# Performance work log

Hardware: AMD Instinct MI355X
Metric: run time of the kernel (lower is better)

The kernel has to match this reference:

```python
import jax, jax.numpy as jnp
import numpy as np

N_FFT = 1024
HOP = 256
WIN = 1024
PAD = (WIN - HOP) // 2  # 'same' padding trim
B, NBINS, T = 32, N_FFT // 2 + 1, 2048


def setup_inputs() -> dict:
    key = jax.random.key(0)
    k1, k2 = jax.random.split(key)
    spec_real = jax.random.normal(k1, (B, NBINS, T), dtype=jnp.float32)
    spec_imag = jax.random.normal(k2, (B, NBINS, T), dtype=jnp.float32)
    # Hann window, as used by neural vocoders (periodic hann)
    n = jnp.arange(WIN, dtype=jnp.float32)
    window = 0.5 - 0.5 * jnp.cos(2.0 * jnp.pi * n / WIN)
    return {"spec_real": spec_real, "spec_imag": spec_imag, "window": window}


def reference(spec_real, spec_imag, window):
    spec = jax.lax.complex(spec_real, spec_imag)            # (B, N, T)
    ifft = jnp.fft.irfft(spec, n=N_FFT, axis=1, norm="backward")  # (B, n_fft, T)
    ifft = ifft * window[None, :, None]                     # windowed frames
    b, _, t = spec_real.shape
    out_size = (t - 1) * HOP + WIN
    idx = jnp.arange(t)[None, :] * HOP + jnp.arange(WIN)[:, None]
    y = jnp.zeros((b, out_size), dtype=ifft.dtype).at[:, idx].add(ifft)
    env = jnp.zeros((out_size,), dtype=window.dtype).at[idx].add(
        jnp.broadcast_to(jnp.square(window)[:, None], (WIN, t))
    )
    return y[:, PAD:-PAD] / env[PAD:-PAD]
```

## Files before the change

kernel.cpp:

```cpp
#include <hip/hip_runtime.h>
#include <hip/hip_fp16.h>

#define NBINS 513
#define TFR   2048
#define NB    32
#define WIN   1024
#define HOP   256
#define PADT  384
#define OPB   524288
#define FR    8
#define TILES (TFR / FR)
#define FSTRIDE 545
#define PIDX(i) ((i) + ((i) >> 4))
#define C45 0.70710678118654752f
#define TWOPI_1024 0.0061359231515425649f
#define SSC   (1.0f / 512.0f * 2.0f / 3.0f)
#define CDLT  0.99998117528260114f
#define SDLT  0.00613588464915448f

__device__ __forceinline__ float2 cadd(float2 a, float2 b){ return make_float2(a.x+b.x, a.y+b.y); }
__device__ __forceinline__ float2 csub(float2 a, float2 b){ return make_float2(a.x-b.x, a.y-b.y); }
__device__ __forceinline__ float2 cmul(float2 a, float2 b){ return make_float2(a.x*b.x - a.y*b.y, a.x*b.y + a.y*b.x); }

__device__ __forceinline__ float2 h2f(__half2 h){ return __half22float2(h); }
__device__ __forceinline__ __half2 f2h(float x, float y){ return __floats2half2_rn(x, y); }

#define BFLY8(u0,u1,u2,u3,u4,u5,u6,u7, v0,v1,v2,v3,v4,v5,v6,v7)            \
    float2 s0=cadd(u0,u4), t0=csub(u0,u4);                                  \
    float2 s1=cadd(u1,u5), t1=csub(u1,u5);                                  \
    float2 s2=cadd(u2,u6), t2=csub(u2,u6);                                  \
    float2 s3=cadd(u3,u7), t3=csub(u3,u7);                                  \
    t1 = make_float2(C45*(t1.x - t1.y),  C45*(t1.x + t1.y));                \
    t2 = make_float2(-t2.y, t2.x);                                          \
    t3 = make_float2(-C45*(t3.x + t3.y), C45*(t3.x - t3.y));                \
    float2 p0=cadd(s0,s2), p2=csub(s0,s2);                                  \
    float2 p1=cadd(s1,s3), p3=csub(s1,s3); p3 = make_float2(-p3.y, p3.x);   \
    float2 q0=cadd(t0,t2), q2=csub(t0,t2);                                  \
    float2 q1=cadd(t1,t3), q3=csub(t1,t3); q3 = make_float2(-q3.y, q3.x);   \
    float2 v0=cadd(p0,p1), v4=csub(p0,p1);                                  \
    float2 v2=cadd(p2,p3), v6=csub(p2,p3);                                  \
    float2 v1=cadd(q0,q1), v5=csub(q0,q1);                                  \
    float2 v3=cadd(q2,q3), v7=csub(q2,q3);

template<int L>
__device__ __forceinline__ void fft_stage(__half2* __restrict__ row,
                                          const float2* __restrict__ ph, int i)
{
    const int k    = i & (L - 1);
    const int base = ((i & ~(L - 1)) << 3) + k;
    float2 u0 = h2f(row[PIDX(base + 0*L)]);
    float2 u1 = h2f(row[PIDX(base + 1*L)]);
    float2 u2 = h2f(row[PIDX(base + 2*L)]);
    float2 u3 = h2f(row[PIDX(base + 3*L)]);
    float2 u4 = h2f(row[PIDX(base + 4*L)]);
    float2 u5 = h2f(row[PIDX(base + 5*L)]);
    float2 u6 = h2f(row[PIDX(base + 6*L)]);
    float2 u7 = h2f(row[PIDX(base + 7*L)]);
    BFLY8(u0,u1,u2,u3,u4,u5,u6,u7, v0,v1,v2,v3,v4,v5,v6,v7)
    if constexpr (L > 1) {
        const float2 w1 = ph[k * (128 / L)];
        float2 wq = w1;
        v1 = cmul(v1, wq);
        wq = cmul(wq, w1); v2 = cmul(v2, wq);
        wq = cmul(wq, w1); v3 = cmul(v3, wq);
        wq = cmul(wq, w1); v4 = cmul(v4, wq);
        wq = cmul(wq, w1); v5 = cmul(v5, wq);
        wq = cmul(wq, w1); v6 = cmul(v6, wq);
        wq = cmul(wq, w1); v7 = cmul(v7, wq);
    }
    row[PIDX(base + 0*L)] = f2h(v0.x, v0.y);
    row[PIDX(base + 1*L)] = f2h(v1.x, v1.y);
    row[PIDX(base + 2*L)] = f2h(v2.x, v2.y);
    row[PIDX(base + 3*L)] = f2h(v3.x, v3.y);
    row[PIDX(base + 4*L)] = f2h(v4.x, v4.y);
    row[PIDX(base + 5*L)] = f2h(v5.x, v5.y);
    row[PIDX(base + 6*L)] = f2h(v6.x, v6.y);
    row[PIDX(base + 7*L)] = f2h(v7.x, v7.y);
}

__device__ __forceinline__ float2 hann_pair(const float2* __restrict__ ph, int n)
{
    const bool mir = n > 256;
    const int  m   = mir ? 512 - n : n;
    const float2 cs = ph[m];
    const float c = mir ? -cs.x : cs.x;
    const float s = cs.y;
    const float w0 = 1.0f - c*c;
    const float c2 = 2.0f*c*c - 1.0f;
    const float s2 = 2.0f*c*s;
    const float w1 = 0.5f - 0.5f*(c2*CDLT - s2*SDLT);
    return make_float2(w0, w1);
}

__global__ __launch_bounds__(256) void zero_seams(float* __restrict__ out)
{
    const int total = NB * 257 * 768;
    for (int id = blockIdx.x * 256 + threadIdx.x; id < total; id += gridDim.x * 256) {
        const int q = id % 768;
        const int r = id / 768;
        const int s = r % 257;
        const int bb = r / 257;
        const int p  = s * 2048 + q;
        const int oi = p - PADT;
        if ((unsigned)oi < (unsigned)OPB) out[(size_t)bb * OPB + oi] = 0.f;
    }
}

__global__ __launch_bounds__(256, 8) void istft8(
    const float* __restrict__ sr, const float* __restrict__ si,
    float* __restrict__ out)
{
    __shared__ __half2 stile[FR * FSTRIDE];
    __shared__ float2  ph[257];

    const int tid = threadIdx.x;
    const int bid = blockIdx.x;
    const int nwg = NB * TILES;
    const int swz = (bid & 7) * (nwg >> 3) + (bid >> 3);
    const int b    = swz / TILES;
    const int tile = swz % TILES;
    const int j0   = tile * FR;

    for (int m = tid; m < 257; m += 256) {
        float sv, cv;
        sincosf(TWOPI_1024 * (float)m, &sv, &cv);
        ph[m] = make_float2(cv, sv);
    }

    const size_t gbase = (size_t)b * NBINS * TFR + (size_t)j0;
    const size_t gaA = gbase + (size_t)tid * TFR;
    const size_t gaB = gbase + (size_t)(512 - tid) * TFR;
    float4 reA0 = *(const float4*)(sr + gaA);
    float4 reA1 = *(const float4*)(sr + gaA + 4);
    float4 imA0 = *(const float4*)(si + gaA);
    float4 imA1 = *(const float4*)(si + gaA + 4);
    float4 reB0 = *(const float4*)(sr + gaB);
    float4 reB1 = *(const float4*)(sr + gaB + 4);
    float4 imB0 = *(const float4*)(si + gaB);
    float4 imB1 = *(const float4*)(si + gaB + 4);
    float4 reC0, reC1, imC0, imC1;
    if (tid == 0) {
        imA0 = imA1 = imB0 = imB1 = make_float4(0.f,0.f,0.f,0.f);
        const size_t gaC = gbase + (size_t)256 * TFR;
        reC0 = *(const float4*)(sr + gaC);
        reC1 = *(const float4*)(sr + gaC + 4);
        imC0 = *(const float4*)(si + gaC);
        imC1 = *(const float4*)(si + gaC + 4);
    }
    __syncthreads();

    {
        const float h = 0.5f * SSC;
        const float2 wt = ph[tid];
        const int pk  = PIDX(tid);
        const int pk2 = PIDX(512 - tid);
#define TRICK(F, XKX, XKY, XMX, XMY) do {                                   \
            const float Ex = h*((XKX)+(XMX)), Ey = h*((XKY)-(XMY));         \
            const float Dx = h*((XKX)-(XMX)), Dy = h*((XKY)+(XMY));         \
            const float Ox = Dx*wt.x - Dy*wt.y, Oy = Dx*wt.y + Dy*wt.x;     \
            stile[(F)*FSTRIDE + pk]  = f2h(Ex - Oy, Ey + Ox);               \
            stile[(F)*FSTRIDE + pk2] = f2h(Ex + Oy, Ox - Ey);               \
        } while (0)
        TRICK(0, reA0.x, imA0.x, reB0.x, imB0.x);
        TRICK(1, reA0.y, imA0.y, reB0.y, imB0.y);
        TRICK(2, reA0.z, imA0.z, reB0.z, imB0.z);
        TRICK(3, reA0.w, imA0.w, reB0.w, imB0.w);
        TRICK(4, reA1.x, imA1.x, reB1.x, imB1.x);
        TRICK(5, reA1.y, imA1.y, reB1.y, imB1.y);
        TRICK(6, reA1.z, imA1.z, reB1.z, imB1.z);
        TRICK(7, reA1.w, imA1.w, reB1.w, imB1.w);
#undef TRICK
        if (tid == 0) {
            const int pn = PIDX(256);
            stile[0*FSTRIDE + pn] = f2h(reC0.x * SSC, -imC0.x * SSC);
            stile[1*FSTRIDE + pn] = f2h(reC0.y * SSC, -imC0.y * SSC);
            stile[2*FSTRIDE + pn] = f2h(reC0.z * SSC, -imC0.z * SSC);
            stile[3*FSTRIDE + pn] = f2h(reC0.w * SSC, -imC0.w * SSC);
            stile[4*FSTRIDE + pn] = f2h(reC1.x * SSC, -imC1.x * SSC);
            stile[5*FSTRIDE + pn] = f2h(reC1.y * SSC, -imC1.y * SSC);
            stile[6*FSTRIDE + pn] = f2h(reC1.z * SSC, -imC1.z * SSC);
            stile[7*FSTRIDE + pn] = f2h(reC1.w * SSC, -imC1.w * SSC);
        }
    }
    __syncthreads();

    {
        const int f  = tid >> 5;
        __half2* row = &stile[f * FSTRIDE];
        const int i0 = tid & 31;
        fft_stage<64>(row, ph, i0);
        fft_stage<64>(row, ph, i0 + 32);
        __syncthreads();
        fft_stage<8>(row, ph, i0);
        fft_stage<8>(row, ph, i0 + 32);
        __syncthreads();
        fft_stage<1>(row, ph, i0);
        fft_stage<1>(row, ph, i0 + 32);
        __syncthreads();
    }

    const int nE = tid;
    const int nO = (tid + 128) & 255;
    const float2 wE0 = hann_pair(ph, nE);
    const float2 wE1 = hann_pair(ph, nE + 256);
    const float2 wO0 = hann_pair(ph, nO);
    const float2 wO1 = hann_pair(ph, nO + 256);

    float2 a0 = make_float2(0.f,0.f), a1 = a0, a2 = a0, a3 = a0, a4 = a0, a5 = a0;
    const bool tlo = (tid < 128);

#define OLA_STEP(F, KK, ACCV, W) do {                                       \
        const int n_ = (((F) & 1) ? nO : nE) + ((KK) << 8);                 \
        const int j_ = ((n_ & 7) << 6) | (n_ & 56) | (n_ >> 6);             \
        const float2 z_ = h2f(stile[(F)*FSTRIDE + PIDX(j_)]);               \
        ACCV.x += z_.x * W.x;                                               \
        ACCV.y += z_.y * W.y;                                               \
    } while (0)

    OLA_STEP(0,0,a0,wE0); OLA_STEP(0,1,a1,wE1);
    if (tlo) { OLA_STEP(1,0,a1,wO0); OLA_STEP(1,1,a2,wO1); }
    else     { OLA_STEP(1,0,a0,wO0); OLA_STEP(1,1,a1,wO1); }
    OLA_STEP(2,0,a1,wE0); OLA_STEP(2,1,a2,wE1);
    if (tlo) { OLA_STEP(3,0,a2,wO0); OLA_STEP(3,1,a3,wO1); }
    else     { OLA_STEP(3,0,a1,wO0); OLA_STEP(3,1,a2,wO1); }
    OLA_STEP(4,0,a2,wE0); OLA_STEP(4,1,a3,wE1);
    if (tlo) { OLA_STEP(5,0,a3,wO0); OLA_STEP(5,1,a4,wO1); }
    else     { OLA_STEP(5,0,a2,wO0); OLA_STEP(5,1,a3,wO1); }
    OLA_STEP(6,0,a3,wE0); OLA_STEP(6,1,a4,wE1);
    if (tlo) { OLA_STEP(7,0,a4,wO0); OLA_STEP(7,1,a5,wO1); }
    else     { OLA_STEP(7,0,a3,wO0); OLA_STEP(7,1,a4,wO1); }
#undef OLA_STEP

    const size_t ob = (size_t)b * OPB;
    const int pb = tile * 2048;
#define STORE_SEAM(A, G) do {                                               \
        const int oi_ = pb + 2*(tid + 256*(G)) - PADT;                      \
        if ((unsigned)oi_ < (unsigned)OPB)       atomicAdd(&out[ob + oi_],     A.x); \
        if ((unsigned)(oi_+1) < (unsigned)OPB)   atomicAdd(&out[ob + oi_ + 1], A.y); \
    } while (0)
#define STORE_PLAIN(A, G) do {                                              \
        const int oi_ = pb + 2*(tid + 256*(G)) - PADT;                      \
        *(float2*)(out + ob + oi_) = A;                                     \
    } while (0)

    STORE_SEAM(a0, 0);
    if (tlo) STORE_SEAM(a1, 1);
    else     STORE_PLAIN(a1, 1);
    STORE_PLAIN(a2, 2);
    STORE_PLAIN(a3, 3);
    STORE_SEAM(a4, 4);
    if (tlo) STORE_SEAM(a5, 5);
#undef STORE_SEAM
#undef STORE_PLAIN
}

__global__ __launch_bounds__(256) void edge_fix(float* __restrict__ out)
{
    const int id = blockIdx.x * 256 + threadIdx.x;
    if (id >= 768 * NB) return;
    const int bb = id / 768;
    const int r  = id % 768;
    const int oi = (r < 384) ? r : (OPB - 768 + r);
    const int p  = oi + PADT;
    int jlo = (p - 768) >> 8; if (jlo < 0) jlo = 0;
    int jhi = p >> 8;         if (jhi > TFR - 1) jhi = TFR - 1;
    float e = 0.f;
    for (int j = jlo; j <= jhi; ++j) {
        const float wv = 0.5f - 0.5f * cosf(TWOPI_1024 * (float)(p - j * HOP));
        e += wv * wv;
    }
    out[(size_t)bb * OPB + oi] *= 1.5f / e;
}

extern "C" void kernel_launch(void* const* d_in, const int* in_sizes, int n_in,
                              void* d_out, int out_size, void* d_ws, size_t ws_size,
                              hipStream_t stream) {
    const float* sr = (const float*)d_in[0];
    const float* si = (const float*)d_in[1];
    float* out = (float*)d_out;

    hipLaunchKernelGGL(zero_seams, dim3(2048), dim3(256), 0, stream, out);
    hipLaunchKernelGGL(istft8, dim3(NB * TILES), dim3(256), 0, stream, sr, si, out);
    hipLaunchKernelGGL(edge_fix, dim3((768 * NB + 255) / 256), dim3(256), 0, stream, out);
}
```

Baseline: 134.4 us.

## Process 16 frames per block to halve seam atomics and tile count

Each workgroup now handles 16 STFT frames instead of 8. The input loads, FFT stage loops and overlap-add chain are extended, and zero_seams and the store pattern are updated so that only the tile boundaries use atomics. The twiddle for the pre-FFT trick is computed with sincosf per thread rather than read from shared memory, which lets the first barrier be dropped. The intent is fewer seam atomicAdds, less seam zeroing and less per-block overhead, at the cost of doubled LDS and registers per block (launch bounds drop to 4 blocks per SM) and twice the per-thread FFT work.

```diff
diff --git a/kernel.cpp b/kernel.cpp
--- a/kernel.cpp
+++ b/kernel.cpp
@@ -8,8 +8,9 @@
 #define HOP   256
 #define PADT  384
 #define OPB   524288
-#define FR    8
+#define FR    16
 #define TILES (TFR / FR)
+#define SPAN  (FR * HOP)
 #define FSTRIDE 545
 #define PIDX(i) ((i) + ((i) >> 4))
 #define C45 0.70710678118654752f
@@ -21,7 +22,6 @@
 __device__ __forceinline__ float2 cadd(float2 a, float2 b){ return make_float2(a.x+b.x, a.y+b.y); }
 __device__ __forceinline__ float2 csub(float2 a, float2 b){ return make_float2(a.x-b.x, a.y-b.y); }
 __device__ __forceinline__ float2 cmul(float2 a, float2 b){ return make_float2(a.x*b.x - a.y*b.y, a.x*b.y + a.y*b.x); }
-
 __device__ __forceinline__ float2 h2f(__half2 h){ return __half22float2(h); }
 __device__ __forceinline__ __half2 f2h(float x, float y){ return __floats2half2_rn(x, y); }
 
@@ -94,19 +94,19 @@
 
 __global__ __launch_bounds__(256) void zero_seams(float* __restrict__ out)
 {
-    const int total = NB * 257 * 768;
+    const int total = NB * (TILES + 1) * 768;
     for (int id = blockIdx.x * 256 + threadIdx.x; id < total; id += gridDim.x * 256) {
         const int q = id % 768;
         const int r = id / 768;
-        const int s = r % 257;
-        const int bb = r / 257;
-        const int p  = s * 2048 + q;
+        const int s = r % (TILES + 1);
+        const int bb = r / (TILES + 1);
+        const int p  = s * SPAN + q;
         const int oi = p - PADT;
         if ((unsigned)oi < (unsigned)OPB) out[(size_t)bb * OPB + oi] = 0.f;
     }
 }
 
-__global__ __launch_bounds__(256, 8) void istft8(
+__global__ __launch_bounds__(256, 4) void istft16(
     const float* __restrict__ sr, const float* __restrict__ si,
     float* __restrict__ out)
 {
@@ -121,81 +121,104 @@
     const int tile = swz % TILES;
     const int j0   = tile * FR;
 
+    const size_t gbase = (size_t)b * NBINS * TFR + (size_t)j0;
+    const size_t gaA = gbase + (size_t)tid * TFR;
+    const size_t gaB = gbase + (size_t)(512 - tid) * TFR;
+    float4 rA0 = *(const float4*)(sr + gaA);
+    float4 rA1 = *(const float4*)(sr + gaA + 4);
+    float4 rA2 = *(const float4*)(sr + gaA + 8);
+    float4 rA3 = *(const float4*)(sr + gaA + 12);
+    float4 iA0 = *(const float4*)(si + gaA);
+    float4 iA1 = *(const float4*)(si + gaA + 4);
+    float4 iA2 = *(const float4*)(si + gaA + 8);
+    float4 iA3 = *(const float4*)(si + gaA + 12);
+    float4 rB0 = *(const float4*)(sr + gaB);
+    float4 rB1 = *(const float4*)(sr + gaB + 4);
+    float4 rB2 = *(const float4*)(sr + gaB + 8);
+    float4 rB3 = *(const float4*)(sr + gaB + 12);
+    float4 iB0 = *(const float4*)(si + gaB);
+    float4 iB1 = *(const float4*)(si + gaB + 4);
+    float4 iB2 = *(const float4*)(si + gaB + 8);
+    float4 iB3 = *(const float4*)(si + gaB + 12);
+
+    if (tid == 0) {
+        const float4 z4 = make_float4(0.f,0.f,0.f,0.f);
+        iA0=iA1=iA2=iA3=z4; iB0=iB1=iB2=iB3=z4;
+        const size_t gaC = gbase + (size_t)256 * TFR;
+        float4 rC0 = *(const float4*)(sr + gaC);
+        float4 rC1 = *(const float4*)(sr + gaC + 4);
+        float4 rC2 = *(const float4*)(sr + gaC + 8);
+        float4 rC3 = *(const float4*)(sr + gaC + 12);
+        float4 iC0 = *(const float4*)(si + gaC);
+        float4 iC1 = *(const float4*)(si + gaC + 4);
+        float4 iC2 = *(const float4*)(si + gaC + 8);
+        float4 iC3 = *(const float4*)(si + gaC + 12);
+        const int pn = PIDX(256);
+#define Z256(F, RC, IC, COMP) stile[(F)*FSTRIDE + pn] = f2h(RC.COMP * SSC, -IC.COMP * SSC)
+        Z256(0,rC0,iC0,x);  Z256(1,rC0,iC0,y);  Z256(2,rC0,iC0,z);  Z256(3,rC0,iC0,w);
+        Z256(4,rC1,iC1,x);  Z256(5,rC1,iC1,y);  Z256(6,rC1,iC1,z);  Z256(7,rC1,iC1,w);
+        Z256(8,rC2,iC2,x);  Z256(9,rC2,iC2,y);  Z256(10,rC2,iC2,z); Z256(11,rC2,iC2,w);
+        Z256(12,rC3,iC3,x); Z256(13,rC3,iC3,y); Z256(14,rC3,iC3,z); Z256(15,rC3,iC3,w);
+#undef Z256
+    }
+
     for (int m = tid; m < 257; m += 256) {
         float sv, cv;
         sincosf(TWOPI_1024 * (float)m, &sv, &cv);
         ph[m] = make_float2(cv, sv);
     }
 
-    const size_t gbase = (size_t)b * NBINS * TFR + (size_t)j0;
-    const size_t gaA = gbase + (size_t)tid * TFR;
-    const size_t gaB = gbase + (size_t)(512 - tid) * TFR;
-    float4 reA0 = *(const float4*)(sr + gaA);
-    float4 reA1 = *(const float4*)(sr + gaA + 4);
-    float4 imA0 = *(const float4*)(si + gaA);
-    float4 imA1 = *(const float4*)(si + gaA + 4);
-    float4 reB0 = *(const float4*)(sr + gaB);
-    float4 reB1 = *(const float4*)(sr + gaB + 4);
-    float4 imB0 = *(const float4*)(si + gaB);
-    float4 imB1 = *(const float4*)(si + gaB + 4);
-    float4 reC0, reC1, imC0, imC1;
-    if (tid == 0) {
-        imA0 = imA1 = imB0 = imB1 = make_float4(0.f,0.f,0.f,0.f);
-        const size_t gaC = gbase + (size_t)256 * TFR;
-        reC0 = *(const float4*)(sr + gaC);
-        reC1 = *(const float4*)(sr + gaC + 4);
-        imC0 = *(const float4*)(si + gaC);
-        imC1 = *(const float4*)(si + gaC + 4);
-    }
-    __syncthreads();
-
     {
         const float h = 0.5f * SSC;
-        const float2 wt = ph[tid];
+        float swt, cwt;
+        sincosf(TWOPI_1024 * (float)tid, &swt, &cwt);
         const int pk  = PIDX(tid);
         const int pk2 = PIDX(512 - tid);
 #define TRICK(F, XKX, XKY, XMX, XMY) do {                                   \
             const float Ex = h*((XKX)+(XMX)), Ey = h*((XKY)-(XMY));         \
             const float Dx = h*((XKX)-(XMX)), Dy = h*((XKY)+(XMY));         \
-            const float Ox = Dx*wt.x - Dy*wt.y, Oy = Dx*wt.y + Dy*wt.x;     \
+            const float Ox = Dx*cwt - Dy*swt, Oy = Dx*swt + Dy*cwt;         \
             stile[(F)*FSTRIDE + pk]  = f2h(Ex - Oy, Ey + Ox);               \
             stile[(F)*FSTRIDE + pk2] = f2h(Ex + Oy, Ox - Ey);               \
         } while (0)
-        TRICK(0, reA0.x, imA0.x, reB0.x, imB0.x);
-        TRICK(1, reA0.y, imA0.y, reB0.y, imB0.y);
-        TRICK(2, reA0.z, imA0.z, reB0.z, imB0.z);
-        TRICK(3, reA0.w, imA0.w, reB0.w, imB0.w);
-        TRICK(4, reA1.x, imA1.x, reB1.x, imB1.x);
-        TRICK(5, reA1.y, imA1.y, reB1.y, imB1.y);
-        TRICK(6, reA1.z, imA1.z, reB1.z, imB1.z);
-        TRICK(7, reA1.w, imA1.w, reB1.w, imB1.w);
+        TRICK(0,  rA0.x, iA0.x, rB0.x, iB0.x);
+        TRICK(1,  rA0.y, iA0.y, rB0.y, iB0.y);
+        TRICK(2,  rA0.z, iA0.z, rB0.z, iB0.z);
+        TRICK(3,  rA0.w, iA0.w, rB0.w, iB0.w);
+        TRICK(4,  rA1.x, iA1.x, rB1.x, iB1.x);
+        TRICK(5,  rA1.y, iA1.y, rB1.y, iB1.y);
+        TRICK(6,  rA1.z, iA1.z, rB1.z, iB1.z);
+        TRICK(7,  rA1.w, iA1.w, rB1.w, iB1.w);
+        TRICK(8,  rA2.x, iA2.x, rB2.x, iB2.x);
+        TRICK(9,  rA2.y, iA2.y, rB2.y, iB2.y);
+        TRICK(10, rA2.z, iA2.z, rB2.z, iB2.z);
+        TRICK(11, rA2.w, iA2.w, rB2.w, iB2.w);
+        TRICK(12, rA3.x, iA3.x, rB3.x, iB3.x);
+        TRICK(13, rA3.y, iA3.y, rB3.y, iB3.y);
+        TRICK(14, rA3.z, iA3.z, rB3.z, iB3.z);
+        TRICK(15, rA3.w, iA3.w, rB3.w, iB3.w);
 #undef TRICK
-        if (tid == 0) {
-            const int pn = PIDX(256);
-            stile[0*FSTRIDE + pn] = f2h(reC0.x * SSC, -imC0.x * SSC);
-            stile[1*FSTRIDE + pn] = f2h(reC0.y * SSC, -imC0.y * SSC);
-            stile[2*FSTRIDE + pn] = f2h(reC0.z * SSC, -imC0.z * SSC);
-            stile[3*FSTRIDE + pn] = f2h(reC0.w * SSC, -imC0.w * SSC);
-            stile[4*FSTRIDE + pn] = f2h(reC1.x * SSC, -imC1.x * SSC);
-            stile[5*FSTRIDE + pn] = f2h(reC1.y * SSC, -imC1.y * SSC);
-            stile[6*FSTRIDE + pn] = f2h(reC1.z * SSC, -imC1.z * SSC);
-            stile[7*FSTRIDE + pn] = f2h(reC1.w * SSC, -imC1.w * SSC);
-        }
     }
     __syncthreads();
 
     {
-        const int f  = tid >> 5;
+        const int f  = tid >> 4;
         __half2* row = &stile[f * FSTRIDE];
-        const int i0 = tid & 31;
+        const int i0 = tid & 15;
         fft_stage<64>(row, ph, i0);
+        fft_stage<64>(row, ph, i0 + 16);
         fft_stage<64>(row, ph, i0 + 32);
+        fft_stage<64>(row, ph, i0 + 48);
         __syncthreads();
         fft_stage<8>(row, ph, i0);
+        fft_stage<8>(row, ph, i0 + 16);
         fft_stage<8>(row, ph, i0 + 32);
+        fft_stage<8>(row, ph, i0 + 48);
         __syncthreads();
         fft_stage<1>(row, ph, i0);
+        fft_stage<1>(row, ph, i0 + 16);
         fft_stage<1>(row, ph, i0 + 32);
+        fft_stage<1>(row, ph, i0 + 48);
         __syncthreads();
     }
 
@@ -206,7 +229,8 @@
     const float2 wO0 = hann_pair(ph, nO);
     const float2 wO1 = hann_pair(ph, nO + 256);
 
-    float2 a0 = make_float2(0.f,0.f), a1 = a0, a2 = a0, a3 = a0, a4 = a0, a5 = a0;
+    float2 a0 = make_float2(0.f,0.f), a1=a0, a2=a0, a3=a0, a4=a0,
+           a5 = a0, a6=a0, a7=a0, a8=a0, a9=a0;
     const bool tlo = (tid < 128);
 
 #define OLA_STEP(F, KK, ACCV, W) do {                                       \
@@ -217,22 +241,34 @@
         ACCV.y += z_.y * W.y;                                               \
     } while (0)
 
-    OLA_STEP(0,0,a0,wE0); OLA_STEP(0,1,a1,wE1);
-    if (tlo) { OLA_STEP(1,0,a1,wO0); OLA_STEP(1,1,a2,wO1); }
-    else     { OLA_STEP(1,0,a0,wO0); OLA_STEP(1,1,a1,wO1); }
-    OLA_STEP(2,0,a1,wE0); OLA_STEP(2,1,a2,wE1);
-    if (tlo) { OLA_STEP(3,0,a2,wO0); OLA_STEP(3,1,a3,wO1); }
-    else     { OLA_STEP(3,0,a1,wO0); OLA_STEP(3,1,a2,wO1); }
-    OLA_STEP(4,0,a2,wE0); OLA_STEP(4,1,a3,wE1);
-    if (tlo) { OLA_STEP(5,0,a3,wO0); OLA_STEP(5,1,a4,wO1); }
-    else     { OLA_STEP(5,0,a2,wO0); OLA_STEP(5,1,a3,wO1); }
-    OLA_STEP(6,0,a3,wE0); OLA_STEP(6,1,a4,wE1);
-    if (tlo) { OLA_STEP(7,0,a4,wO0); OLA_STEP(7,1,a5,wO1); }
-    else     { OLA_STEP(7,0,a3,wO0); OLA_STEP(7,1,a4,wO1); }
+    OLA_STEP(0,0,a0,wE0);  OLA_STEP(0,1,a1,wE1);
+    if (tlo) { OLA_STEP(1,0,a1,wO0);  OLA_STEP(1,1,a2,wO1); }
+    else     { OLA_STEP(1,0,a0,wO0);  OLA_STEP(1,1,a1,wO1); }
+    OLA_STEP(2,0,a1,wE0);  OLA_STEP(2,1,a2,wE1);
+    if (tlo) { OLA_STEP(3,0,a2,wO0);  OLA_STEP(3,1,a3,wO1); }
+    else     { OLA_STEP(3,0,a1,wO0);  OLA_STEP(3,1,a2,wO1); }
+    OLA_STEP(4,0,a2,wE0);  OLA_STEP(4,1,a3,wE1);
+    if (tlo) { OLA_STEP(5,0,a3,wO0);  OLA_STEP(5,1,a4,wO1); }
+    else     { OLA_STEP(5,0,a2,wO0);  OLA_STEP(5,1,a3,wO1); }
+    OLA_STEP(6,0,a3,wE0);  OLA_STEP(6,1,a4,wE1);
+    if (tlo) { OLA_STEP(7,0,a4,wO0);  OLA_STEP(7,1,a5,wO1); }
+    else     { OLA_STEP(7,0,a3,wO0);  OLA_STEP(7,1,a4,wO1); }
+    OLA_STEP(8,0,a4,wE0);  OLA_STEP(8,1,a5,wE1);
+    if (tlo) { OLA_STEP(9,0,a5,wO0);  OLA_STEP(9,1,a6,wO1); }
+    else     { OLA_STEP(9,0,a4,wO0);  OLA_STEP(9,1,a5,wO1); }
+    OLA_STEP(10,0,a5,wE0); OLA_STEP(10,1,a6,wE1);
+    if (tlo) { OLA_STEP(11,0,a6,wO0); OLA_STEP(11,1,a7,wO1); }
+    else     { OLA_STEP(11,0,a5,wO0); OLA_STEP(11,1,a6,wO1); }
+    OLA_STEP(12,0,a6,wE0); OLA_STEP(12,1,a7,wE1);
+    if (tlo) { OLA_STEP(13,0,a7,wO0); OLA_STEP(13,1,a8,wO1); }
+    else     { OLA_STEP(13,0,a6,wO0); OLA_STEP(13,1,a7,wO1); }
+    OLA_STEP(14,0,a7,wE0); OLA_STEP(14,1,a8,wE1);
+    if (tlo) { OLA_STEP(15,0,a8,wO0); OLA_STEP(15,1,a9,wO1); }
+    else     { OLA_STEP(15,0,a7,wO0); OLA_STEP(15,1,a8,wO1); }
 #undef OLA_STEP
 
     const size_t ob = (size_t)b * OPB;
-    const int pb = tile * 2048;
+    const int pb = tile * SPAN;
 #define STORE_SEAM(A, G) do {                                               \
         const int oi_ = pb + 2*(tid + 256*(G)) - PADT;                      \
         if ((unsigned)oi_ < (unsigned)OPB)       atomicAdd(&out[ob + oi_],     A.x); \
@@ -248,8 +284,12 @@
     else     STORE_PLAIN(a1, 1);
     STORE_PLAIN(a2, 2);
     STORE_PLAIN(a3, 3);
-    STORE_SEAM(a4, 4);
-    if (tlo) STORE_SEAM(a5, 5);
+    STORE_PLAIN(a4, 4);
+    STORE_PLAIN(a5, 5);
+    STORE_PLAIN(a6, 6);
+    STORE_PLAIN(a7, 7);
+    STORE_SEAM(a8, 8);
+    if (tlo) STORE_SEAM(a9, 9);
 #undef STORE_SEAM
 #undef STORE_PLAIN
 }
@@ -280,6 +320,6 @@
     float* out = (float*)d_out;
 
     hipLaunchKernelGGL(zero_seams, dim3(2048), dim3(256), 0, stream, out);
-    hipLaunchKernelGGL(istft8, dim3(NB * TILES), dim3(256), 0, stream, sr, si, out);
+    hipLaunchKernelGGL(istft16, dim3(NB * TILES), dim3(256), 0, stream, sr, si, out);
     hipLaunchKernelGGL(edge_fix, dim3((768 * NB + 255) / 256), dim3(256), 0, stream, out);
 }
```

New measurement: 109.9 us. 1.22x faster.
